# Kernel tuning notes

Measured on AMD Instinct MI355X. Metric: run time of the kernel, lower is better.

## Reference

```python
import jax, jax.numpy as jnp
import numpy as np

CHANNELS = 512
NUM_HEADS = 4
GROUPS = 32
EPS = 1e-5


def setup_inputs() -> dict:
    key = jax.random.key(0)
    ks = jax.random.split(key, 7)
    C = CHANNELS
    x = jax.random.normal(ks[0], (16, C, 32, 32), dtype=jnp.float32)
    norm_w = jnp.ones((C,), dtype=jnp.float32)
    norm_b = jnp.zeros((C,), dtype=jnp.float32)
    qkv_w = jax.random.normal(ks[1], (3 * C, C), dtype=jnp.float32) * (C ** -0.5)
    qkv_b = jnp.zeros((3 * C,), dtype=jnp.float32)
    proj_w = jax.random.normal(ks[2], (C, C), dtype=jnp.float32) * (C ** -0.5)
    proj_b = jnp.zeros((C,), dtype=jnp.float32)
    return {"x": x, "norm_w": norm_w, "norm_b": norm_b,
            "qkv_w": qkv_w, "qkv_b": qkv_b,
            "proj_w": proj_w, "proj_b": proj_b}


def reference(x, norm_w, norm_b, qkv_w, qkv_b, proj_w, proj_b):
    B, C, H, W = x.shape
    heads = NUM_HEADS
    hd = C // heads  # head dim
    N = H * W

    # GroupNorm(32, C): normalize over (C/32, H, W) per group, then per-channel affine
    xg = x.reshape(B, GROUPS, -1)
    mu = jnp.mean(xg, axis=-1, keepdims=True)
    var = jnp.var(xg, axis=-1, keepdims=True)
    h = ((xg - mu) * jax.lax.rsqrt(var + EPS)).reshape(B, C, H, W)
    h = h * norm_w[None, :, None, None] + norm_b[None, :, None, None]

    # 1x1 conv qkv: [B,C,H,W] -> [B,3C,H,W]
    qkv = jnp.einsum('oc,bchw->bohw', qkv_w, h) + qkv_b[None, :, None, None]
    qkv = qkv.reshape(B, 3, heads, hd, N)
    q, k, v = qkv[:, 0], qkv[:, 1], qkv[:, 2]  # each [B, heads, hd, N]

    scale = hd ** -0.5
    attn = jnp.einsum('bhcn,bhcm->bhnm', q, k) * scale  # [B, heads, N, N]
    attn = jax.nn.softmax(attn, axis=-1)
    h = jnp.einsum('bhnm,bhcm->bhcn', attn, v).reshape(B, C, H, W)

    # 1x1 conv proj + residual
    h = jnp.einsum('oc,bchw->bohw', proj_w, h) + proj_b[None, :, None, None]
    return x + h
```

## Files before the change

kernel.cpp:

```cpp
#include <hip/hip_runtime.h>

typedef __bf16 v8bf __attribute__((ext_vector_type(8)));
typedef float  v4f  __attribute__((ext_vector_type(4)));
typedef float  v16f __attribute__((ext_vector_type(16)));
typedef unsigned short u16;

__device__ __forceinline__ u16 f2bf(float f){
  __bf16 h = (__bf16)f;
  union { __bf16 h; u16 u; } c; c.h = h; return c.u;
}
__device__ __forceinline__ v4f v4zero(){ v4f z; z[0]=0.f; z[1]=0.f; z[2]=0.f; z[3]=0.f; return z; }

#define MFMA16(a,b,c) __builtin_amdgcn_mfma_f32_16x16x32_bf16((a),(b),(c),0,0,0)
#define MFMA32(a,b,c) __builtin_amdgcn_mfma_f32_32x32x16_bf16((a),(b),(c),0,0,0)

__device__ __forceinline__ void gl_lds16(const u16* g, u16* l){
  __builtin_amdgcn_global_load_lds((const __attribute__((address_space(1))) void*)g,
                                   (__attribute__((address_space(3))) void*)l, 16, 0, 0);
}

__device__ __forceinline__ unsigned int pkbf(float lo, float hi){
  unsigned int r;
  asm("v_cvt_pk_bf16_f32 %0, %1, %2" : "=v"(r) : "v"(lo), "v"(hi));
  return r;
}

__global__ __launch_bounds__(256) void cvt2_kernel(const float* __restrict__ a, u16* __restrict__ da, int na,
                                                   const float* __restrict__ b, u16* __restrict__ db, int nb){
  int i = (blockIdx.x*256 + threadIdx.x)*4;
  const float* s; u16* d; int off;
  if (i < na){ s = a; d = da; off = i; }
  else { off = i - na; if (off >= nb) return; s = b; d = db; }
  float4 v = *(const float4*)(s + off);
  ushort4 o;
  o.x = f2bf(v.x); o.y = f2bf(v.y); o.z = f2bf(v.z); o.w = f2bf(v.w);
  *(ushort4*)(d + off) = o;
}

__global__ __launch_bounds__(256) void gn_fused_kernel(const float* __restrict__ x, const float* __restrict__ nw,
                                                       const float* __restrict__ nb, u16* __restrict__ h_t){
  __shared__ float xs[16*1028 + 16];
  const int bg = blockIdx.x, b = bg >> 5, g = bg & 31, c0 = g*16;
  const int tid = threadIdx.x;
  const float* base = x + (size_t)(b*512 + c0)*1024;

  float s = 0.f, ss = 0.f;
  #pragma unroll
  for (int it = 0; it < 16; ++it){
    float4 v = *(const float4*)(base + it*1024 + tid*4);
    s  += v.x + v.y + v.z + v.w;
    ss += v.x*v.x + v.y*v.y + v.z*v.z + v.w*v.w;
    *(float4*)(xs + it*1028 + tid*4) = v;
  }
  #pragma unroll
  for (int off = 32; off > 0; off >>= 1){ s += __shfl_down(s, off); ss += __shfl_down(ss, off); }
  float* red = xs + 16*1028;
  int w = tid >> 6;
  if ((tid & 63) == 0){ red[w] = s; red[4+w] = ss; }
  __syncthreads();
  if (tid == 0){
    float S  = red[0]+red[1]+red[2]+red[3];
    float SS = red[4]+red[5]+red[6]+red[7];
    float mean = S * (1.f/16384.f);
    float var  = SS * (1.f/16384.f) - mean*mean;
    red[8] = mean;
    red[9] = rsqrtf(var + 1e-5f);
  }
  __syncthreads();
  const float mean = red[8], rstd = red[9];

  const int half = tid & 1, nbase = tid >> 1;
  float wv[8], bv[8];
  #pragma unroll
  for (int cl = 0; cl < 8; ++cl){
    int c = c0 + half*8 + cl;
    wv[cl] = nw[c] * rstd;
    bv[cl] = nb[c] - mean * wv[cl];
  }
  #pragma unroll
  for (int p = 0; p < 8; ++p){
    int n = nbase + p*128;
    alignas(16) u16 tmp[8];
    #pragma unroll
    for (int cl = 0; cl < 8; ++cl)
      tmp[cl] = f2bf(xs[(half*8 + cl)*1028 + n] * wv[cl] + bv[cl]);
    *(int4*)(h_t + ((size_t)b*1024 + n)*512 + c0 + half*8) = *(int4*)tmp;
  }
}

__global__ __launch_bounds__(256,2) void gemm_qkv_kernel(
    const u16* __restrict__ A,
    const u16* __restrict__ B,
    const float* __restrict__ bias,
    u16* __restrict__ qk_t, u16* __restrict__ v_ws)
{
  __shared__ u16 smem[24576];
  const int tid = threadIdx.x, w = tid>>6, lane = tid&63, col = lane&15, quad = lane>>4;
  const int m0 = blockIdx.y*128;
  const int n0 = blockIdx.x*256;
  const int b  = blockIdx.z;
  const int lr = lane>>2;
  const int gsw = ((lane&3) ^ (lr&3))*8;
  const u16* Ag = A + ((size_t)b*1024 + m0 + w*32 + lr)*512 + gsw;
  const u16* Bg = B + (size_t)(n0 + w*64 + lr)*512 + gsw;
  const int mw = (w&1)*64, nw = (w>>1)*128;
  const int fsw = (quad ^ (col&3))*8;

  v4f acc[4][8];
  #pragma unroll
  for (int i=0;i<4;++i)
    #pragma unroll
    for (int j=0;j<8;++j) acc[i][j] = v4zero();

  {
    u16* Ab = smem + (w*32)*32;
    u16* Bb = smem + 4096 + (w*64)*32;
    #pragma unroll
    for (int p = 0; p < 2; ++p) gl_lds16(Ag + (size_t)(p*16)*512, Ab + p*512);
    #pragma unroll
    for (int p = 0; p < 4; ++p) gl_lds16(Bg + (size_t)(p*16)*512, Bb + p*512);
  }

  for (int kt = 0; kt < 16; ++kt){
    __syncthreads();
    if (kt < 15){
      u16* Ab = smem + ((kt+1)&1)*12288 + (w*32)*32;
      u16* Bb = smem + ((kt+1)&1)*12288 + 4096 + (w*64)*32;
      int ko = (kt+1)*32;
      #pragma unroll
      for (int p = 0; p < 2; ++p) gl_lds16(Ag + (size_t)(p*16)*512 + ko, Ab + p*512);
      #pragma unroll
      for (int p = 0; p < 4; ++p) gl_lds16(Bg + (size_t)(p*16)*512 + ko, Bb + p*512);
    }
    const u16* As = smem + (kt&1)*12288;
    const u16* Bs = As + 4096;
    v8bf a[4], bb[8];
    #pragma unroll
    for (int i = 0; i < 4; ++i) a[i]  = *(const v8bf*)(As + (mw+i*16+col)*32 + fsw);
    #pragma unroll
    for (int j = 0; j < 8; ++j) bb[j] = *(const v8bf*)(Bs + (nw+j*16+col)*32 + fsw);
    #pragma unroll
    for (int i = 0; i < 4; ++i)
      #pragma unroll
      for (int j = 0; j < 8; ++j)
        acc[i][j] = MFMA16(a[i], bb[j], acc[i][j]);
  }
  __syncthreads();

  float bc[8];
  #pragma unroll
  for (int j = 0; j < 8; ++j)
    bc[j] = bias[n0 + nw + j*16 + col];

  if (n0 < 1024){
    u16* Cs = smem + w*(64*72);
    #pragma unroll
    for (int half = 0; half < 2; ++half){
      #pragma unroll
      for (int i = 0; i < 4; ++i)
        #pragma unroll
        for (int jj = 0; jj < 4; ++jj)
          #pragma unroll
          for (int r = 0; r < 4; ++r)
            Cs[(i*16+quad*4+r)*72 + jj*16+col] = f2bf(acc[i][half*4+jj][r] + bc[half*4+jj]);
      u16* dst = qk_t + (size_t)b*1024*1024;
      #pragma unroll
      for (int p = 0; p < 8; ++p){
        int rl = p*8 + (lane>>3), cl = (lane&7)*8;
        *(int4*)(dst + (size_t)(m0+mw+rl)*1024 + n0+nw+half*64+cl) = *(int4*)(Cs + rl*72 + cl);
      }
    }
  } else {
    u16* Ct = smem + w*(64*80);
    #pragma unroll
    for (int half = 0; half < 2; ++half){
      #pragma unroll
      for (int i = 0; i < 4; ++i)
        #pragma unroll
        for (int jj = 0; jj < 4; ++jj)
          #pragma unroll
          for (int r = 0; r < 4; ++r)
            Ct[(jj*16+col)*80 + i*16+quad*4+r] = f2bf(acc[i][half*4+jj][r] + bc[half*4+jj]);
      u16* dst = v_ws + (size_t)b*512*1024;
      #pragma unroll
      for (int p = 0; p < 8; ++p){
        int rl = p*8 + (lane>>3), cl = (lane&7)*8;
        *(int4*)(dst + (size_t)(n0-1024 + nw + half*64 + rl)*1024 + m0+mw+cl) = *(int4*)(Ct + rl*80 + cl);
      }
    }
  }
}

__global__ __launch_bounds__(256,2) void gemm_bt_kernel(
    const u16* __restrict__ A, long long sA,
    const u16* __restrict__ B, long long sB,
    u16* __restrict__ Cbf, float* __restrict__ Cf, long long sC,
    const float* __restrict__ bias_row,
    const float* __restrict__ bias_col,
    const float* __restrict__ residf, long long sR,
    int M, int N, int K)
{
  __shared__ u16 smem[32768];
  const int tid = threadIdx.x, w = tid>>6, lane = tid&63, col = lane&15, quad = lane>>4;
  const int m0 = blockIdx.y*128, n0 = blockIdx.x*128;
  const int lr8 = lane>>3;
  const int gsw = ((lane&7) ^ lr8)*8;
  const u16* Ag = A + (size_t)blockIdx.z*sA + (size_t)(m0 + w*32 + lr8)*K + gsw;
  const u16* Bg = B + (size_t)blockIdx.z*sB + (size_t)(n0 + w*32 + lr8)*K + gsw;
  const int mw = (w&1)*64, nw = (w>>1)*64;
  const int csw = col&7;
  const int nt = K >> 6;

  v4f acc[4][4];
  #pragma unroll
  for (int i=0;i<4;++i)
    #pragma unroll
    for (int j=0;j<4;++j) acc[i][j] = v4zero();

  {
    u16* Ab = smem + (w*32)*64;
    u16* Bb = smem + 8192 + (w*32)*64;
    #pragma unroll
    for (int p = 0; p < 4; ++p){
      gl_lds16(Ag + (size_t)(p*8)*K, Ab + p*512);
      gl_lds16(Bg + (size_t)(p*8)*K, Bb + p*512);
    }
  }

  for (int kt = 0; kt < nt; ++kt){
    __syncthreads();
    if (kt+1 < nt){
      u16* Ab = smem + ((kt+1)&1)*16384 + (w*32)*64;
      u16* Bb = smem + ((kt+1)&1)*16384 + 8192 + (w*32)*64;
      int ko = (kt+1)*64;
      #pragma unroll
      for (int p = 0; p < 4; ++p){
        gl_lds16(Ag + (size_t)(p*8)*K + ko, Ab + p*512);
        gl_lds16(Bg + (size_t)(p*8)*K + ko, Bb + p*512);
      }
    }
    const u16* As = smem + (kt&1)*16384;
    const u16* Bs = As + 8192;
    #pragma unroll
    for (int kh = 0; kh < 2; ++kh){
      const int fs = ((kh*4 + quad) ^ csw)*8;
      v8bf a[4], bb[4];
      #pragma unroll
      for (int i = 0; i < 4; ++i) a[i]  = *(const v8bf*)(As + (mw+i*16+col)*64 + fs);
      #pragma unroll
      for (int j = 0; j < 4; ++j) bb[j] = *(const v8bf*)(Bs + (nw+j*16+col)*64 + fs);
      #pragma unroll
      for (int i = 0; i < 4; ++i)
        #pragma unroll
        for (int j = 0; j < 4; ++j)
          acc[i][j] = MFMA16(a[i], bb[j], acc[i][j]);
    }
  }
  __syncthreads();

  float br[4][4], bc[4];
  #pragma unroll
  for (int i = 0; i < 4; ++i)
    #pragma unroll
    for (int r = 0; r < 4; ++r)
      br[i][r] = bias_row ? bias_row[m0+mw+i*16+quad*4+r] : 0.f;
  #pragma unroll
  for (int j = 0; j < 4; ++j)
    bc[j] = bias_col ? bias_col[n0+nw+j*16+col] : 0.f;

  if (Cf){
    float* Cb = Cf + (size_t)blockIdx.z*sC;
    const float* Rb = residf ? residf + (size_t)blockIdx.z*sR : nullptr;
    #pragma unroll
    for (int i = 0; i < 4; ++i)
      #pragma unroll
      for (int r = 0; r < 4; ++r){
        int row = m0+mw+i*16+quad*4+r;
        #pragma unroll
        for (int j = 0; j < 4; ++j){
          size_t goff = (size_t)row*N + n0+nw+j*16+col;
          float val = acc[i][j][r] + br[i][r] + bc[j];
          if (Rb) val += Rb[goff];
          Cb[goff] = val;
        }
      }
  } else {
    u16* Cs = smem + w*(64*72);
    #pragma unroll
    for (int i = 0; i < 4; ++i)
      #pragma unroll
      for (int j = 0; j < 4; ++j)
        #pragma unroll
        for (int r = 0; r < 4; ++r)
          Cs[(i*16+quad*4+r)*72 + j*16+col] = f2bf(acc[i][j][r] + br[i][r] + bc[j]);
    __syncthreads();
    u16* Cb = Cbf + (size_t)blockIdx.z*sC;
    #pragma unroll
    for (int p = 0; p < 8; ++p){
      int rl = p*8 + (lane>>3), cl = (lane&7)*8;
      size_t goff = (size_t)(m0+mw+rl)*N + n0+nw+cl;
      *(int4*)(Cb + goff) = *(int4*)(Cs + rl*72 + cl);
    }
  }
}

__global__ __launch_bounds__(256,2) void attn_kernel(const u16* __restrict__ qk, const u16* __restrict__ vv,
                                                     u16* __restrict__ outp){
  __shared__ u16 smem[32768];
  u16* Ks = smem;
  u16* Vs = smem + 16384;
  const int id = blockIdx.x;
  const int qt = id >> 6, bh = id & 63, b = bh >> 2, h = bh & 3;
  const int n0 = qt*128;
  const int tid = threadIdx.x, w = tid>>6, lane = tid&63;
  const int nl = lane & 31, hi = lane >> 5;
  const int key = nl & 7;
  const size_t bq = (size_t)b*1024*1024;
  const float scale2 = 0.12751742f;

  v8bf qf[8];
  {
    const u16* qbase = qk + bq + (size_t)(n0 + w*32 + nl)*1024 + h*128 + hi*8;
    #pragma unroll
    for (int kk = 0; kk < 8; ++kk)
      qf[kk] = *(const v8bf*)(qbase + kk*16);
  }

  v16f o[4];
  #pragma unroll
  for (int j=0;j<4;++j)
    #pragma unroll
    for (int r=0;r<16;++r) o[j][r] = 0.f;
  float lsum = 0.f;

  const int krow = w*4 + (lane>>4);
  const int kgr  = (lane&15) ^ (krow&7);
  const u16* kg_base = qk + bq + (size_t)krow*1024 + 512 + h*128 + kgr*8;
  const int vrow = w*8 + (lane>>3);
  const int vgr  = (lane&7) ^ (vrow&7);
  const u16* vg_base = vv + ((size_t)b*512 + h*128 + vrow)*1024 + vgr*8;

  #pragma unroll
  for (int p = 0; p < 4; ++p)
    gl_lds16(kg_base + (size_t)(p*16)*1024, Ks + (w*4)*128 + p*2048);
  #pragma unroll
  for (int p = 0; p < 4; ++p)
    gl_lds16(vg_base + (size_t)(p*32)*1024, Vs + (w*8)*64 + p*2048);

  for (int t = 0; t < 16; ++t){
    const int mt = t*64;
    __syncthreads();

    if (t < 15){
      int mt2 = mt + 64;
      u16* kl = Ks + (((t+1)&1)<<13) + (w*4)*128;
      #pragma unroll
      for (int p = 0; p < 4; ++p)
        gl_lds16(kg_base + (size_t)(mt2 + p*16)*1024, kl + p*2048);
      u16* vl = Vs + (((t+1)&1)<<13) + (w*8)*64;
      #pragma unroll
      for (int p = 0; p < 4; ++p)
        gl_lds16(vg_base + (size_t)(p*32)*1024 + mt2, vl + p*2048);
    }

    const u16* Kc = Ks + ((t&1)<<13);
    v16f s0, s1;
    #pragma unroll
    for (int r=0;r<16;++r){ s0[r]=0.f; s1[r]=0.f; }
    __builtin_amdgcn_s_setprio(1);
    #pragma unroll
    for (int kk = 0; kk < 8; ++kk){
      int g = (((kk*2 + hi) ^ key) << 3);
      v8bf k0 = *(const v8bf*)(Kc + (nl<<7) + g);
      v8bf k1 = *(const v8bf*)(Kc + ((32+nl)<<7) + g);
      s0 = MFMA32(k0, qf[kk], s0);
      s1 = MFMA32(k1, qf[kk], s1);
    }
    __builtin_amdgcn_s_setprio(0);

    #pragma unroll
    for (int r = 0; r < 16; ++r){
      s0[r] = __builtin_amdgcn_exp2f(s0[r]*scale2);
      s1[r] = __builtin_amdgcn_exp2f(s1[r]*scale2);
      lsum += s0[r] + s1[r];
    }

    const u16* Vc = Vs + ((t&1)<<13);
    #pragma unroll
    for (int half = 0; half < 2; ++half){
      const v16f& ps = half ? s1 : s0;
      #pragma unroll
      for (int sel = 0; sel < 2; ++sel){
        const int sb = sel*8;
        unsigned int pA = pkbf(ps[sb+0], ps[sb+1]);
        unsigned int pB = pkbf(ps[sb+2], ps[sb+3]);
        unsigned int pC = pkbf(ps[sb+4], ps[sb+5]);
        unsigned int pD = pkbf(ps[sb+6], ps[sb+7]);
        asm("v_permlane32_swap_b32 %0, %1" : "+v"(pA), "+v"(pC));
        asm("v_permlane32_swap_b32 %0, %1" : "+v"(pB), "+v"(pD));
        union { v8bf v; unsigned int u[4]; } pa;
        pa.u[0] = pA; pa.u[1] = pB; pa.u[2] = pC; pa.u[3] = pD;
        const int kkv = half*2 + sel;
        const int gv = (((kkv*2 + hi) ^ key) << 3);
        __builtin_amdgcn_s_setprio(1);
        #pragma unroll
        for (int j = 0; j < 4; ++j){
          v8bf bv = *(const v8bf*)(Vc + ((j*32 + nl)<<6) + gv);
          o[j] = MFMA32(pa.v, bv, o[j]);
        }
        __builtin_amdgcn_s_setprio(0);
      }
    }
  }
  __syncthreads();

  lsum += __shfl_xor(lsum, 32);
  float invl[16];
  #pragma unroll
  for (int r = 0; r < 16; ++r){
    int nr = (r&3) + 8*(r>>2) + 4*hi;
    invl[r] = 1.f / __shfl(lsum, nr);
  }

  #pragma unroll
  for (int j = 0; j < 4; ++j)
    #pragma unroll
    for (int r = 0; r < 16; ++r){
      int rr = w*32 + (r&3) + 8*(r>>2) + 4*hi;
      int c  = j*32 + nl;
      smem[(rr<<7) + ((((c>>3) ^ (rr&7))<<3)) + (c&7)] = f2bf(o[j][r] * invl[r]);
    }
  __syncthreads();
  #pragma unroll
  for (int p = 0; p < 8; ++p){
    int nr = p*16 + (tid>>4);
    int gc = (tid&15) ^ (nr&7);
    *(int4*)(outp + ((size_t)b*1024 + n0 + nr)*512 + h*128 + ((tid&15)<<3)) =
      *(int4*)(smem + (nr<<7) + (gc<<3));
  }
}

extern "C" void kernel_launch(void* const* d_in, const int* in_sizes, int n_in,
                              void* d_out, int out_size, void* d_ws, size_t ws_size,
                              hipStream_t stream){
  const float* x      = (const float*)d_in[0];
  const float* norm_w = (const float*)d_in[1];
  const float* norm_b = (const float*)d_in[2];
  const float* qkv_w  = (const float*)d_in[3];
  const float* qkv_b  = (const float*)d_in[4];
  const float* proj_w = (const float*)d_in[5];
  const float* proj_b = (const float*)d_in[6];
  float* out = (float*)d_out;

  u16* h_t   = (u16*)d_ws;
  u16* qk_t  = h_t  + (size_t)16*1024*512;
  u16* v_ws  = qk_t + (size_t)16*1024*1024;
  u16* wq_bf = v_ws + (size_t)16*512*1024;
  u16* wp_bf = wq_bf + (size_t)1536*512;
  u16* attnout = h_t;

  cvt2_kernel<<<1024, 256, 0, stream>>>(qkv_w, wq_bf, 1536*512, proj_w, wp_bf, 512*512);
  gn_fused_kernel<<<512, 256, 0, stream>>>(x, norm_w, norm_b, h_t);

  gemm_qkv_kernel<<<dim3(6,8,16), 256, 0, stream>>>(h_t, wq_bf, qkv_b, qk_t, v_ws);

  attn_kernel<<<512, 256, 0, stream>>>(qk_t, v_ws, attnout);

  gemm_bt_kernel<<<dim3(8,4,16), 256, 0, stream>>>(
      wp_bf, 0, attnout, (long long)1024*512,
      nullptr, out, (long long)512*1024, proj_b, nullptr, x, (long long)512*1024, 512, 1024, 512);
}
```

Measured before the change: 206.9 us.

## Process two query sub-tiles per wave in attention to reuse K/V fragments

The attention kernel now runs 2 waves (128 threads) per block instead of 4, and each wave handles 64 query rows as two 32-row sub-tiles. Every K and V fragment read from LDS feeds two MFMAs, which halves LDS reads per FLOP. The load and store loops are reshaped to cover the same tiles with fewer threads. The cost is much higher register pressure (two accumulator sets and two Q fragment sets), fewer waves per block, and launch bounds of (128,1), all of which may reduce latency hiding.

```diff
diff --git a/kernel.cpp b/kernel.cpp
--- a/kernel.cpp
+++ b/kernel.cpp
@@ -304,7 +304,7 @@
   }
 }
 
-__global__ __launch_bounds__(256,2) void attn_kernel(const u16* __restrict__ qk, const u16* __restrict__ vv,
+__global__ __launch_bounds__(128,1) void attn_kernel(const u16* __restrict__ qk, const u16* __restrict__ vv,
                                                      u16* __restrict__ outp){
   __shared__ u16 smem[32768];
   u16* Ks = smem;
@@ -318,20 +318,21 @@
   const size_t bq = (size_t)b*1024*1024;
   const float scale2 = 0.12751742f;
 
-  v8bf qf[8];
-  {
-    const u16* qbase = qk + bq + (size_t)(n0 + w*32 + nl)*1024 + h*128 + hi*8;
+  v8bf qf[2][8];
+  #pragma unroll
+  for (int u = 0; u < 2; ++u){
+    const u16* qbase = qk + bq + (size_t)(n0 + w*64 + u*32 + nl)*1024 + h*128 + hi*8;
     #pragma unroll
     for (int kk = 0; kk < 8; ++kk)
-      qf[kk] = *(const v8bf*)(qbase + kk*16);
-  }
-
-  v16f o[4];
+      qf[u][kk] = *(const v8bf*)(qbase + kk*16);
+  }
+
+  v16f o0[4], o1[4];
   #pragma unroll
   for (int j=0;j<4;++j)
     #pragma unroll
-    for (int r=0;r<16;++r) o[j][r] = 0.f;
-  float lsum = 0.f;
+    for (int r=0;r<16;++r){ o0[j][r] = 0.f; o1[j][r] = 0.f; }
+  float l0a = 0.f, l0b = 0.f, l1a = 0.f, l1b = 0.f;
 
   const int krow = w*4 + (lane>>4);
   const int kgr  = (lane&15) ^ (krow&7);
@@ -341,11 +342,11 @@
   const u16* vg_base = vv + ((size_t)b*512 + h*128 + vrow)*1024 + vgr*8;
 
   #pragma unroll
-  for (int p = 0; p < 4; ++p)
-    gl_lds16(kg_base + (size_t)(p*16)*1024, Ks + (w*4)*128 + p*2048);
-  #pragma unroll
-  for (int p = 0; p < 4; ++p)
-    gl_lds16(vg_base + (size_t)(p*32)*1024, Vs + (w*8)*64 + p*2048);
+  for (int p = 0; p < 8; ++p)
+    gl_lds16(kg_base + (size_t)(p*8)*1024, Ks + (w*4)*128 + p*1024);
+  #pragma unroll
+  for (int p = 0; p < 8; ++p)
+    gl_lds16(vg_base + (size_t)(p*16)*1024, Vs + (w*8)*64 + p*1024);
 
   for (int t = 0; t < 16; ++t){
     const int mt = t*64;
@@ -355,58 +356,72 @@
       int mt2 = mt + 64;
       u16* kl = Ks + (((t+1)&1)<<13) + (w*4)*128;
       #pragma unroll
-      for (int p = 0; p < 4; ++p)
-        gl_lds16(kg_base + (size_t)(mt2 + p*16)*1024, kl + p*2048);
+      for (int p = 0; p < 8; ++p)
+        gl_lds16(kg_base + (size_t)(mt2 + p*8)*1024, kl + p*1024);
       u16* vl = Vs + (((t+1)&1)<<13) + (w*8)*64;
       #pragma unroll
-      for (int p = 0; p < 4; ++p)
-        gl_lds16(vg_base + (size_t)(p*32)*1024 + mt2, vl + p*2048);
+      for (int p = 0; p < 8; ++p)
+        gl_lds16(vg_base + (size_t)(p*16)*1024 + mt2, vl + p*1024);
     }
 
     const u16* Kc = Ks + ((t&1)<<13);
-    v16f s0, s1;
-    #pragma unroll
-    for (int r=0;r<16;++r){ s0[r]=0.f; s1[r]=0.f; }
+    v16f s0a, s0b, s1a, s1b;
+    #pragma unroll
+    for (int r=0;r<16;++r){ s0a[r]=0.f; s0b[r]=0.f; s1a[r]=0.f; s1b[r]=0.f; }
     __builtin_amdgcn_s_setprio(1);
     #pragma unroll
     for (int kk = 0; kk < 8; ++kk){
       int g = (((kk*2 + hi) ^ key) << 3);
       v8bf k0 = *(const v8bf*)(Kc + (nl<<7) + g);
       v8bf k1 = *(const v8bf*)(Kc + ((32+nl)<<7) + g);
-      s0 = MFMA32(k0, qf[kk], s0);
-      s1 = MFMA32(k1, qf[kk], s1);
+      s0a = MFMA32(k0, qf[0][kk], s0a);
+      s0b = MFMA32(k1, qf[0][kk], s0b);
+      s1a = MFMA32(k0, qf[1][kk], s1a);
+      s1b = MFMA32(k1, qf[1][kk], s1b);
     }
     __builtin_amdgcn_s_setprio(0);
 
     #pragma unroll
     for (int r = 0; r < 16; ++r){
-      s0[r] = __builtin_amdgcn_exp2f(s0[r]*scale2);
-      s1[r] = __builtin_amdgcn_exp2f(s1[r]*scale2);
-      lsum += s0[r] + s1[r];
+      s0a[r] = __builtin_amdgcn_exp2f(s0a[r]*scale2);
+      s0b[r] = __builtin_amdgcn_exp2f(s0b[r]*scale2);
+      s1a[r] = __builtin_amdgcn_exp2f(s1a[r]*scale2);
+      s1b[r] = __builtin_amdgcn_exp2f(s1b[r]*scale2);
+      l0a += s0a[r]; l0b += s0b[r];
+      l1a += s1a[r]; l1b += s1b[r];
     }
 
     const u16* Vc = Vs + ((t&1)<<13);
     #pragma unroll
     for (int half = 0; half < 2; ++half){
-      const v16f& ps = half ? s1 : s0;
+      const v16f& p0 = half ? s0b : s0a;
+      const v16f& p1 = half ? s1b : s1a;
       #pragma unroll
       for (int sel = 0; sel < 2; ++sel){
         const int sb = sel*8;
-        unsigned int pA = pkbf(ps[sb+0], ps[sb+1]);
-        unsigned int pB = pkbf(ps[sb+2], ps[sb+3]);
-        unsigned int pC = pkbf(ps[sb+4], ps[sb+5]);
-        unsigned int pD = pkbf(ps[sb+6], ps[sb+7]);
-        asm("v_permlane32_swap_b32 %0, %1" : "+v"(pA), "+v"(pC));
-        asm("v_permlane32_swap_b32 %0, %1" : "+v"(pB), "+v"(pD));
-        union { v8bf v; unsigned int u[4]; } pa;
-        pa.u[0] = pA; pa.u[1] = pB; pa.u[2] = pC; pa.u[3] = pD;
+        unsigned int pA0 = pkbf(p0[sb+0], p0[sb+1]);
+        unsigned int pB0 = pkbf(p0[sb+2], p0[sb+3]);
+        unsigned int pC0 = pkbf(p0[sb+4], p0[sb+5]);
+        unsigned int pD0 = pkbf(p0[sb+6], p0[sb+7]);
+        asm("v_permlane32_swap_b32 %0, %1" : "+v"(pA0), "+v"(pC0));
+        asm("v_permlane32_swap_b32 %0, %1" : "+v"(pB0), "+v"(pD0));
+        unsigned int pA1 = pkbf(p1[sb+0], p1[sb+1]);
+        unsigned int pB1 = pkbf(p1[sb+2], p1[sb+3]);
+        unsigned int pC1 = pkbf(p1[sb+4], p1[sb+5]);
+        unsigned int pD1 = pkbf(p1[sb+6], p1[sb+7]);
+        asm("v_permlane32_swap_b32 %0, %1" : "+v"(pA1), "+v"(pC1));
+        asm("v_permlane32_swap_b32 %0, %1" : "+v"(pB1), "+v"(pD1));
+        union { v8bf v; unsigned int u[4]; } pa0, pa1;
+        pa0.u[0] = pA0; pa0.u[1] = pB0; pa0.u[2] = pC0; pa0.u[3] = pD0;
+        pa1.u[0] = pA1; pa1.u[1] = pB1; pa1.u[2] = pC1; pa1.u[3] = pD1;
         const int kkv = half*2 + sel;
         const int gv = (((kkv*2 + hi) ^ key) << 3);
         __builtin_amdgcn_s_setprio(1);
         #pragma unroll
         for (int j = 0; j < 4; ++j){
           v8bf bv = *(const v8bf*)(Vc + ((j*32 + nl)<<6) + gv);
-          o[j] = MFMA32(pa.v, bv, o[j]);
+          o0[j] = MFMA32(pa0.v, bv, o0[j]);
+          o1[j] = MFMA32(pa1.v, bv, o1[j]);
         }
         __builtin_amdgcn_s_setprio(0);
       }
@@ -414,26 +429,31 @@
   }
   __syncthreads();
 
-  lsum += __shfl_xor(lsum, 32);
-  float invl[16];
+  float l0 = l0a + l0b; l0 += __shfl_xor(l0, 32);
+  float l1 = l1a + l1b; l1 += __shfl_xor(l1, 32);
+  float invl0[16], invl1[16];
   #pragma unroll
   for (int r = 0; r < 16; ++r){
     int nr = (r&3) + 8*(r>>2) + 4*hi;
-    invl[r] = 1.f / __shfl(lsum, nr);
+    invl0[r] = 1.f / __shfl(l0, nr);
+    invl1[r] = 1.f / __shfl(l1, nr);
   }
 
   #pragma unroll
   for (int j = 0; j < 4; ++j)
     #pragma unroll
     for (int r = 0; r < 16; ++r){
-      int rr = w*32 + (r&3) + 8*(r>>2) + 4*hi;
+      int rloc = (r&3) + 8*(r>>2) + 4*hi;
       int c  = j*32 + nl;
-      smem[(rr<<7) + ((((c>>3) ^ (rr&7))<<3)) + (c&7)] = f2bf(o[j][r] * invl[r]);
-    }
-  __syncthreads();
-  #pragma unroll
-  for (int p = 0; p < 8; ++p){
-    int nr = p*16 + (tid>>4);
+      int rr0 = w*64 + rloc;
+      smem[(rr0<<7) + ((((c>>3) ^ (rr0&7))<<3)) + (c&7)] = f2bf(o0[j][r] * invl0[r]);
+      int rr1 = w*64 + 32 + rloc;
+      smem[(rr1<<7) + ((((c>>3) ^ (rr1&7))<<3)) + (c&7)] = f2bf(o1[j][r] * invl1[r]);
+    }
+  __syncthreads();
+  #pragma unroll
+  for (int p = 0; p < 16; ++p){
+    int nr = p*8 + (tid>>4);
     int gc = (tid&15) ^ (nr&7);
     *(int4*)(outp + ((size_t)b*1024 + n0 + nr)*512 + h*128 + ((tid&15)<<3)) =
       *(int4*)(smem + (nr<<7) + (gc<<3));
@@ -464,7 +484,7 @@
 
   gemm_qkv_kernel<<<dim3(6,8,16), 256, 0, stream>>>(h_t, wq_bf, qkv_b, qk_t, v_ws);
 
-  attn_kernel<<<512, 256, 0, stream>>>(qk_t, v_ws, attnout);
+  attn_kernel<<<512, 128, 0, stream>>>(qk_t, v_ws, attnout);
 
   gemm_bt_kernel<<<dim3(8,4,16), 256, 0, stream>>>(
       wp_bf, 0, attnout, (long long)1024*512,
```

After: 214.7 us. 1.04x slower.

## Load K tiles directly from global into registers instead of via LDS

Applied to the files above, without the earlier changes.

K tiles for the QK^T MFMA are no longer staged through double-buffered shared memory. Each lane now loads its K fragments straight from global memory into registers, prefetching the next tile after the current MFMAs are issued. This halves LDS usage, which could raise occupancy, and removes the LDS reads for K. The cost is higher register pressure (16 extra v8bf per lane) and global K loads that are redundant across the four waves and less coalesced.

```diff
diff --git a/kernel.cpp b/kernel.cpp
--- a/kernel.cpp
+++ b/kernel.cpp
@@ -306,9 +306,8 @@
 
 __global__ __launch_bounds__(256,2) void attn_kernel(const u16* __restrict__ qk, const u16* __restrict__ vv,
                                                      u16* __restrict__ outp){
-  __shared__ u16 smem[32768];
-  u16* Ks = smem;
-  u16* Vs = smem + 16384;
+  __shared__ u16 smem[16384];
+  u16* Vs = smem;
   const int id = blockIdx.x;
   const int qt = id >> 6, bh = id & 63, b = bh >> 2, h = bh & 3;
   const int n0 = qt*128;
@@ -326,6 +325,8 @@
       qf[kk] = *(const v8bf*)(qbase + kk*16);
   }
 
+  const u16* kbase = qk + bq + (size_t)nl*1024 + 512 + h*128 + hi*8;
+
   v16f o[4];
   #pragma unroll
   for (int j=0;j<4;++j)
@@ -333,50 +334,50 @@
     for (int r=0;r<16;++r) o[j][r] = 0.f;
   float lsum = 0.f;
 
-  const int krow = w*4 + (lane>>4);
-  const int kgr  = (lane&15) ^ (krow&7);
-  const u16* kg_base = qk + bq + (size_t)krow*1024 + 512 + h*128 + kgr*8;
   const int vrow = w*8 + (lane>>3);
   const int vgr  = (lane&7) ^ (vrow&7);
   const u16* vg_base = vv + ((size_t)b*512 + h*128 + vrow)*1024 + vgr*8;
 
   #pragma unroll
   for (int p = 0; p < 4; ++p)
-    gl_lds16(kg_base + (size_t)(p*16)*1024, Ks + (w*4)*128 + p*2048);
-  #pragma unroll
-  for (int p = 0; p < 4; ++p)
     gl_lds16(vg_base + (size_t)(p*32)*1024, Vs + (w*8)*64 + p*2048);
+  v8bf kX[8], kY[8];
+  #pragma unroll
+  for (int kk = 0; kk < 8; ++kk){
+    kX[kk] = *(const v8bf*)(kbase + kk*16);
+    kY[kk] = *(const v8bf*)(kbase + (size_t)32*1024 + kk*16);
+  }
 
   for (int t = 0; t < 16; ++t){
-    const int mt = t*64;
     __syncthreads();
 
     if (t < 15){
-      int mt2 = mt + 64;
-      u16* kl = Ks + (((t+1)&1)<<13) + (w*4)*128;
-      #pragma unroll
-      for (int p = 0; p < 4; ++p)
-        gl_lds16(kg_base + (size_t)(mt2 + p*16)*1024, kl + p*2048);
+      int mt2 = t*64 + 64;
       u16* vl = Vs + (((t+1)&1)<<13) + (w*8)*64;
       #pragma unroll
       for (int p = 0; p < 4; ++p)
         gl_lds16(vg_base + (size_t)(p*32)*1024 + mt2, vl + p*2048);
     }
 
-    const u16* Kc = Ks + ((t&1)<<13);
     v16f s0, s1;
     #pragma unroll
     for (int r=0;r<16;++r){ s0[r]=0.f; s1[r]=0.f; }
     __builtin_amdgcn_s_setprio(1);
     #pragma unroll
     for (int kk = 0; kk < 8; ++kk){
-      int g = (((kk*2 + hi) ^ key) << 3);
-      v8bf k0 = *(const v8bf*)(Kc + (nl<<7) + g);
-      v8bf k1 = *(const v8bf*)(Kc + ((32+nl)<<7) + g);
-      s0 = MFMA32(k0, qf[kk], s0);
-      s1 = MFMA32(k1, qf[kk], s1);
+      s0 = MFMA32(kX[kk], qf[kk], s0);
+      s1 = MFMA32(kY[kk], qf[kk], s1);
     }
     __builtin_amdgcn_s_setprio(0);
+
+    if (t < 15){
+      const u16* kt = kbase + (size_t)(t*64 + 64)*1024;
+      #pragma unroll
+      for (int kk = 0; kk < 8; ++kk){
+        kX[kk] = *(const v8bf*)(kt + kk*16);
+        kY[kk] = *(const v8bf*)(kt + (size_t)32*1024 + kk*16);
+      }
+    }
 
     #pragma unroll
     for (int r = 0; r < 16; ++r){
```

Result: slower. 235.2 us (+13.7%).

## Software-pipeline attention: overlap previous tile's PV MFMAs with current QK MFMAs

Applied to the files above, without the earlier changes.

Restructures the attention main loop so the P·V matrix multiplies for tile t-1 are interleaved with the Q·K^T MFMAs for tile t. The exp/softmax work then overlaps with tensor work instead of serializing. V gets triple buffering in LDS, which grows shared memory from 64KB to 80KB, because the previous V tile must stay live while the next one is loaded. This adds register pressure from the packed P fragments and more LDS per block, which at two blocks per CU could reduce occupancy or cause spills.

```diff
diff --git a/kernel.cpp b/kernel.cpp
--- a/kernel.cpp
+++ b/kernel.cpp
@@ -24,6 +24,24 @@
   asm("v_cvt_pk_bf16_f32 %0, %1, %2" : "=v"(r) : "v"(lo), "v"(hi));
   return r;
 }
+
+#define PACK8(ps, base, dst) { \
+  unsigned int pA = pkbf((ps)[(base)+0], (ps)[(base)+1]); \
+  unsigned int pB = pkbf((ps)[(base)+2], (ps)[(base)+3]); \
+  unsigned int pC = pkbf((ps)[(base)+4], (ps)[(base)+5]); \
+  unsigned int pD = pkbf((ps)[(base)+6], (ps)[(base)+7]); \
+  asm("v_permlane32_swap_b32 %0, %1" : "+v"(pA), "+v"(pC)); \
+  asm("v_permlane32_swap_b32 %0, %1" : "+v"(pB), "+v"(pD)); \
+  union { v8bf v; unsigned int u[4]; } pu; \
+  pu.u[0]=pA; pu.u[1]=pB; pu.u[2]=pC; pu.u[3]=pD; \
+  (dst) = pu.v; }
+
+#define PVBLK(kkv, pa) { \
+  const int gv_ = ((((kkv)*2 + hi) ^ key) << 3); \
+  _Pragma("unroll") \
+  for (int j_ = 0; j_ < 4; ++j_){ \
+    v8bf bv_ = *(const v8bf*)(Vprev + ((j_*32 + nl)<<6) + gv_); \
+    o[j_] = MFMA32((pa), bv_, o[j_]); } }
 
 __global__ __launch_bounds__(256) void cvt2_kernel(const float* __restrict__ a, u16* __restrict__ da, int na,
                                                    const float* __restrict__ b, u16* __restrict__ db, int nb){
@@ -306,7 +324,7 @@
 
 __global__ __launch_bounds__(256,2) void attn_kernel(const u16* __restrict__ qk, const u16* __restrict__ vv,
                                                      u16* __restrict__ outp){
-  __shared__ u16 smem[32768];
+  __shared__ u16 smem[40960];
   u16* Ks = smem;
   u16* Vs = smem + 16384;
   const int id = blockIdx.x;
@@ -347,23 +365,22 @@
   for (int p = 0; p < 4; ++p)
     gl_lds16(vg_base + (size_t)(p*32)*1024, Vs + (w*8)*64 + p*2048);
 
-  for (int t = 0; t < 16; ++t){
-    const int mt = t*64;
-    __syncthreads();
-
-    if (t < 15){
-      int mt2 = mt + 64;
-      u16* kl = Ks + (((t+1)&1)<<13) + (w*4)*128;
-      #pragma unroll
-      for (int p = 0; p < 4; ++p)
-        gl_lds16(kg_base + (size_t)(mt2 + p*16)*1024, kl + p*2048);
-      u16* vl = Vs + (((t+1)&1)<<13) + (w*8)*64;
-      #pragma unroll
-      for (int p = 0; p < 4; ++p)
-        gl_lds16(vg_base + (size_t)(p*32)*1024 + mt2, vl + p*2048);
-    }
-
-    const u16* Kc = Ks + ((t&1)<<13);
+  v8bf ppA, ppB, ppC, ppD;
+  const u16* Vprev = Vs;
+  int vb = 0;
+
+  __syncthreads();
+  {
+    u16* kl = Ks + (1<<13) + (w*4)*128;
+    #pragma unroll
+    for (int p = 0; p < 4; ++p)
+      gl_lds16(kg_base + (size_t)(64 + p*16)*1024, kl + p*2048);
+    u16* vl = Vs + (1<<13) + (w*8)*64;
+    #pragma unroll
+    for (int p = 0; p < 4; ++p)
+      gl_lds16(vg_base + (size_t)(p*32)*1024 + 64, vl + p*2048);
+
+    const u16* Kc = Ks;
     v16f s0, s1;
     #pragma unroll
     for (int r=0;r<16;++r){ s0[r]=0.f; s1[r]=0.f; }
@@ -377,41 +394,65 @@
       s1 = MFMA32(k1, qf[kk], s1);
     }
     __builtin_amdgcn_s_setprio(0);
-
     #pragma unroll
     for (int r = 0; r < 16; ++r){
       s0[r] = __builtin_amdgcn_exp2f(s0[r]*scale2);
       s1[r] = __builtin_amdgcn_exp2f(s1[r]*scale2);
       lsum += s0[r] + s1[r];
     }
-
-    const u16* Vc = Vs + ((t&1)<<13);
-    #pragma unroll
-    for (int half = 0; half < 2; ++half){
-      const v16f& ps = half ? s1 : s0;
-      #pragma unroll
-      for (int sel = 0; sel < 2; ++sel){
-        const int sb = sel*8;
-        unsigned int pA = pkbf(ps[sb+0], ps[sb+1]);
-        unsigned int pB = pkbf(ps[sb+2], ps[sb+3]);
-        unsigned int pC = pkbf(ps[sb+4], ps[sb+5]);
-        unsigned int pD = pkbf(ps[sb+6], ps[sb+7]);
-        asm("v_permlane32_swap_b32 %0, %1" : "+v"(pA), "+v"(pC));
-        asm("v_permlane32_swap_b32 %0, %1" : "+v"(pB), "+v"(pD));
-        union { v8bf v; unsigned int u[4]; } pa;
-        pa.u[0] = pA; pa.u[1] = pB; pa.u[2] = pC; pa.u[3] = pD;
-        const int kkv = half*2 + sel;
-        const int gv = (((kkv*2 + hi) ^ key) << 3);
-        __builtin_amdgcn_s_setprio(1);
-        #pragma unroll
-        for (int j = 0; j < 4; ++j){
-          v8bf bv = *(const v8bf*)(Vc + ((j*32 + nl)<<6) + gv);
-          o[j] = MFMA32(pa.v, bv, o[j]);
-        }
-        __builtin_amdgcn_s_setprio(0);
-      }
-    }
-  }
+    PACK8(s0, 0, ppA); PACK8(s0, 8, ppB); PACK8(s1, 0, ppC); PACK8(s1, 8, ppD);
+  }
+  vb = 1;
+
+  for (int t = 1; t < 16; ++t){
+    __syncthreads();
+    int vbn = vb + 1; if (vbn == 3) vbn = 0;
+    if (t < 15){
+      int mt2 = t*64 + 64;
+      u16* kl = Ks + (((t+1)&1)<<13) + (w*4)*128;
+      #pragma unroll
+      for (int p = 0; p < 4; ++p)
+        gl_lds16(kg_base + (size_t)(mt2 + p*16)*1024, kl + p*2048);
+      u16* vl = Vs + (vbn<<13) + (w*8)*64;
+      #pragma unroll
+      for (int p = 0; p < 4; ++p)
+        gl_lds16(vg_base + (size_t)(p*32)*1024 + mt2, vl + p*2048);
+    }
+
+    const u16* Kc = Ks + ((t&1)<<13);
+    v16f s0, s1;
+    #pragma unroll
+    for (int r=0;r<16;++r){ s0[r]=0.f; s1[r]=0.f; }
+    __builtin_amdgcn_s_setprio(1);
+    #pragma unroll
+    for (int kk = 0; kk < 8; ++kk){
+      int g = (((kk*2 + hi) ^ key) << 3);
+      v8bf k0 = *(const v8bf*)(Kc + (nl<<7) + g);
+      v8bf k1 = *(const v8bf*)(Kc + ((32+nl)<<7) + g);
+      s0 = MFMA32(k0, qf[kk], s0);
+      s1 = MFMA32(k1, qf[kk], s1);
+      if (kk == 1){ PVBLK(0, ppA); }
+      if (kk == 3){ PVBLK(1, ppB); }
+      if (kk == 5){ PVBLK(2, ppC); }
+      if (kk == 7){ PVBLK(3, ppD); }
+    }
+    __builtin_amdgcn_s_setprio(0);
+
+    #pragma unroll
+    for (int r = 0; r < 16; ++r){
+      s0[r] = __builtin_amdgcn_exp2f(s0[r]*scale2);
+      s1[r] = __builtin_amdgcn_exp2f(s1[r]*scale2);
+      lsum += s0[r] + s1[r];
+    }
+    PACK8(s0, 0, ppA); PACK8(s0, 8, ppB); PACK8(s1, 0, ppC); PACK8(s1, 8, ppD);
+
+    Vprev = Vs + (vb<<13);
+    vb = vbn;
+  }
+
+  __builtin_amdgcn_s_setprio(1);
+  PVBLK(0, ppA); PVBLK(1, ppB); PVBLK(2, ppC); PVBLK(3, ppD);
+  __builtin_amdgcn_s_setprio(0);
   __syncthreads();
 
   lsum += __shfl_xor(lsum, 32);
```

Measured after the change: 203.1 us. About the same (-1.9%).
